# Optimization experiments

Hardware: AMD Instinct MI355X
Metric: run time of the kernel (lower is better)

Reference implementation:

```python
import jax, jax.numpy as jnp
import numpy as np

D_MODEL = 1024
NUM_HEADS = 16
D_KEY = D_MODEL // NUM_HEADS


def setup_inputs() -> dict:
    key = jax.random.key(0)
    ks = jax.random.split(key, 9)
    s = 1.0 / np.sqrt(D_MODEL)
    inp = {
        "x": jax.random.normal(ks[0], (4, 2048, D_MODEL), dtype=jnp.float32),
        "Wq": jax.random.uniform(ks[1], (D_MODEL, D_MODEL), jnp.float32, -s, s),
        "bq": jax.random.uniform(ks[2], (D_MODEL,), jnp.float32, -s, s),
        "Wk": jax.random.uniform(ks[3], (D_MODEL, D_MODEL), jnp.float32, -s, s),
        "bk": jax.random.uniform(ks[4], (D_MODEL,), jnp.float32, -s, s),
        "Wv": jax.random.uniform(ks[5], (D_MODEL, D_MODEL), jnp.float32, -s, s),
        "bv": jax.random.uniform(ks[6], (D_MODEL,), jnp.float32, -s, s),
        "Wo": jax.random.uniform(ks[7], (D_MODEL, D_MODEL), jnp.float32, -s, s),
        "bo": jax.random.uniform(ks[8], (D_MODEL,), jnp.float32, -s, s),
    }
    return inp


def reference(x, Wq, bq, Wk, bk, Wv, bv, Wo, bo):
    B, S, D = x.shape
    H, Dk = NUM_HEADS, D_KEY
    # QKV projections (torch Linear: x @ W.T + b; here W stored as [in,out])
    q = (x @ Wq + bq).reshape(B, S, H, Dk).transpose(0, 2, 1, 3)  # [B,H,S,Dk]
    k = (x @ Wk + bk).reshape(B, S, H, Dk).transpose(0, 2, 1, 3)
    v = (x @ Wv + bv).reshape(B, S, H, Dk).transpose(0, 2, 1, 3)
    logits = jnp.einsum("bhqd,bhkd->bhqk", q, k) / jnp.sqrt(jnp.float32(Dk))
    causal = jnp.triu(jnp.ones((S, S), dtype=bool), k=1)  # True above diagonal
    logits = jnp.where(causal, -jnp.inf, logits)
    attn = jax.nn.softmax(logits, axis=-1)
    out = jnp.einsum("bhqk,bhkd->bhqd", attn, v)  # [B,H,S,Dk]
    out = out.transpose(0, 2, 1, 3).reshape(B, S, D)
    return out @ Wo + bo
```

## Files before the change

### kernel.cpp

```cpp
#include <hip/hip_runtime.h>
#include <hip/hip_bf16.h>

#define DEVI __device__ __forceinline__

typedef __attribute__((ext_vector_type(8))) __bf16 bf16x8;
typedef __attribute__((ext_vector_type(4))) float f32x4;
typedef __attribute__((ext_vector_type(16))) float f32x16;
typedef __attribute__((ext_vector_type(8))) unsigned short ushort8;
typedef __attribute__((ext_vector_type(4))) int i32x4;

constexpr int D_MODEL = 1024;
constexpr int NHEAD   = 16;
constexpr int SEQ     = 2048;
constexpr int BATCH   = 4;
constexpr int MTOK    = BATCH * SEQ;

DEVI unsigned short f2bf(float x) {
  __hip_bfloat16 h = __float2bfloat16(x);
  return __builtin_bit_cast(unsigned short, h);
}

DEVI bf16x8 ld_bf8(const unsigned short* p) {
  ushort8 u = *reinterpret_cast<const ushort8*>(p);
  return __builtin_bit_cast(bf16x8, u);
}

DEVI void gload_lds16(const void* g, void* l) {
  __builtin_amdgcn_global_load_lds(
      (const __attribute__((address_space(1))) void*)g,
      (__attribute__((address_space(3))) void*)l, 16, 0, 0);
}

DEVI int cvtpk(float a, float b) {
  int r;
  asm("v_cvt_pk_bf16_f32 %0, %1, %2" : "=v"(r) : "v"(a), "v"(b));
  return r;
}
DEVI void pswap(int& a, int& b) {
  asm volatile("v_permlane32_swap_b32 %0, %1" : "+v"(a), "+v"(b));
}
DEVI float xhalf_sum(float x) { return x + __shfl_xor(x, 32, 64); }

DEVI float tree16sum(const float* p) {
  float a = p[0] + p[1], b = p[2] + p[3], c = p[4] + p[5], d = p[6] + p[7];
  float e = p[8] + p[9], f = p[10] + p[11], g = p[12] + p[13], h = p[14] + p[15];
  a += b; c += d; e += f; g += h;
  return (a + c) + (e + g);
}
DEVI bf16x8 mk_frag(const float* p, int off) {
  int w0 = cvtpk(p[off + 0], p[off + 1]);
  int w1 = cvtpk(p[off + 2], p[off + 3]);
  int w2 = cvtpk(p[off + 4], p[off + 5]);
  int w3 = cvtpk(p[off + 6], p[off + 7]);
  pswap(w0, w2);
  pswap(w1, w3);
  i32x4 v{w0, w1, w2, w3};
  return __builtin_bit_cast(bf16x8, v);
}

__global__ void prep_kernel(const float* __restrict__ x, unsigned short* __restrict__ xb,
                            const float* __restrict__ Wq, const float* __restrict__ Wk,
                            const float* __restrict__ Wv, const float* __restrict__ Wo,
                            unsigned short* __restrict__ Wtq, unsigned short* __restrict__ Wtk,
                            unsigned short* __restrict__ Wtv, unsigned short* __restrict__ Wto) {
  const int z = blockIdx.z;
  if (z >= 4) {
    const int bid = (z - 4) * 256 + blockIdx.y * 16 + blockIdx.x;
    const float4* in4 = reinterpret_cast<const float4*>(x);
    ushort4* out4 = reinterpret_cast<ushort4*>(xb);
#pragma unroll
    for (int j = 0; j < 16; ++j) {
      const int i4 = bid * 4096 + j * 256 + threadIdx.x;
      float4 v = in4[i4];
      ushort4 o;
      o.x = f2bf(v.x); o.y = f2bf(v.y); o.z = f2bf(v.z); o.w = f2bf(v.w);
      out4[i4] = o;
    }
    return;
  }
  __shared__ float tile[64][65];
  const float* W = z == 0 ? Wq : z == 1 ? Wk : z == 2 ? Wv : Wo;
  unsigned short* Wt = z == 0 ? Wtq : z == 1 ? Wtk : z == 2 ? Wtv : Wto;
  const int k0 = blockIdx.x * 64, n0 = blockIdx.y * 64;
  const int tx = threadIdx.x & 63, ty = threadIdx.x >> 6;
  for (int r = ty; r < 64; r += 4)
    tile[r][tx] = W[(size_t)(k0 + r) * D_MODEL + n0 + tx];
  __syncthreads();
  for (int r = ty; r < 64; r += 4)
    Wt[(size_t)(n0 + r) * D_MODEL + k0 + tx] = f2bf(tile[tx][r]);
}

__global__ __launch_bounds__(256) void gemm128(
    const unsigned short* __restrict__ A,
    const unsigned short* __restrict__ Bt,
    const float* __restrict__ bias,
    void* __restrict__ outp, int mode, float scale) {
  constexpr int K = 1024, N = 1024, KT = K / 64;
  __shared__ __align__(16) unsigned short As[2][128 * 64];
  __shared__ __align__(16) unsigned short Bs[2][128 * 64];
  const int t = threadIdx.x;
  const int w = t >> 6, l = t & 63;
  const int bid2 = ((blockIdx.x & 7) << 6) | (blockIdx.x >> 3);
  const int bm = bid2 >> 3, bn = bid2 & 7;
  const int m0 = bm * 128, n0 = bn * 128;
  const int wm = (w >> 1) * 64, wn = (w & 1) * 64;
  const int lr = l & 15, lg = l >> 4;

  f32x4 acc[4][4] = {};

  auto stage = [&](int kt, int buf) {
    const int k0 = kt * 64;
#pragma unroll
    for (int p = 0; p < 4; ++p) {
      const int seg = p * 4 + w;
      const int row = seg * 8 + (l >> 3);
      const int c = (l & 7) ^ (row & 7);
      gload_lds16(A + (size_t)(m0 + row) * K + k0 + c * 8, &As[buf][seg * 512]);
      gload_lds16(Bt + (size_t)(n0 + row) * K + k0 + c * 8, &Bs[buf][seg * 512]);
    }
  };

  stage(0, 0);
  __syncthreads();

  for (int kt = 0; kt < KT; ++kt) {
    const int cur = kt & 1;
    if (kt + 1 < KT) {
      stage(kt + 1, cur ^ 1);
      asm volatile("s_waitcnt vmcnt(8)" ::: "memory");
    } else {
      asm volatile("s_waitcnt vmcnt(0)" ::: "memory");
    }
    __builtin_amdgcn_sched_barrier(0);
    __builtin_amdgcn_s_barrier();
#pragma unroll
    for (int ks = 0; ks < 2; ++ks) {
      bf16x8 af[4], bfr[4];
      const int kk = lg + ks * 4;
#pragma unroll
      for (int i = 0; i < 4; ++i) {
        const int rowA = wm + i * 16 + lr;
        af[i] = ld_bf8(&As[cur][rowA * 64 + ((kk ^ (rowA & 7)) * 8)]);
        const int rowB = wn + i * 16 + lr;
        bfr[i] = ld_bf8(&Bs[cur][rowB * 64 + ((kk ^ (rowB & 7)) * 8)]);
      }
#pragma unroll
      for (int mi = 0; mi < 4; ++mi)
#pragma unroll
        for (int ni = 0; ni < 4; ++ni)
          acc[mi][ni] = __builtin_amdgcn_mfma_f32_16x16x32_bf16(
              af[mi], bfr[ni], acc[mi][ni], 0, 0, 0);
    }
    __builtin_amdgcn_sched_barrier(0);
    __builtin_amdgcn_s_barrier();
  }

#pragma unroll
  for (int ni = 0; ni < 4; ++ni) {
    const int n = n0 + wn + ni * 16 + lr;
    const float bv = bias[n];
#pragma unroll
    for (int mi = 0; mi < 4; ++mi) {
#pragma unroll
      for (int r = 0; r < 4; ++r) {
        const int m = m0 + wm + mi * 16 + lg * 4 + r;
        const float v = (acc[mi][ni][r] + bv) * scale;
        if (mode == 2) {
          ((float*)outp)[(size_t)m * N + n] = v;
        } else {
          const int b = m >> 11, s = m & 2047, h = n >> 6, dk = n & 63;
          unsigned short* o = (unsigned short*)outp;
          if (mode == 0)
            o[(((size_t)(b * NHEAD + h) * SEQ + s) << 6) + dk] = f2bf(v);
          else
            o[(((size_t)(b * NHEAD + h) << 6) + dk) * SEQ + s] = f2bf(v);
        }
      }
    }
  }
}

__global__ __launch_bounds__(256) void attn_kernel(
    const unsigned short* __restrict__ Q,
    const unsigned short* __restrict__ Kt,
    const unsigned short* __restrict__ Vt,
    unsigned short* __restrict__ Oa) {
  __shared__ __align__(16) unsigned short Ks[2][64 * 64];
  __shared__ __align__(16) unsigned short Vs[2][64 * 64];
  const int t = threadIdx.x, w = t >> 6, l = t & 63;
  const int bid = blockIdx.x;
  const int tix = bid >> 6;
  const int tk = tix >> 2, tg = tix & 3;
  const int qt = tk == 0 ? 15 - tg : tk == 1 ? 8 + tg : tk == 2 ? 4 + tg : 3 - tg;
  const int bh = bid & 63;
  const int l31 = l & 31, hi = l >> 5;
  const int jcnt = 2 * qt + 2;
  const int q0w = qt * 128 + w * 32;
  const int qg = q0w + l31;

  const unsigned short* Qb = Q + ((size_t)bh * SEQ + qg) * 64;
  bf16x8 qf[4];
#pragma unroll
  for (int ks = 0; ks < 4; ++ks)
    qf[ks] = ld_bf8(Qb + ks * 16 + hi * 8);

  f32x16 psum = {};
  f32x16 oacc[2] = {};

  auto stage = [&](int jtile, int buf) {
#pragma unroll
    for (int i = 0; i < 2; ++i) {
      const int seg = w * 2 + i;
      const int row = seg * 8 + (l >> 3);
      const int cg = (l & 7) ^ (row & 7);
      gload_lds16(Kt + (((size_t)bh * SEQ + jtile * 64 + row) << 6) + cg * 8,
                  &Ks[buf][seg * 512]);
      gload_lds16(Vt + ((size_t)bh * 64 + row) * SEQ + jtile * 64 + cg * 8,
                  &Vs[buf][seg * 512]);
    }
  };

  stage(0, 0);
  __syncthreads();

  for (int jt = 0; jt < jcnt; ++jt) {
    const int cur = jt & 1;
    if (jt + 1 < jcnt) {
      stage(jt + 1, cur ^ 1);
      asm volatile("s_waitcnt vmcnt(4)" ::: "memory");
    } else {
      asm volatile("s_waitcnt vmcnt(0)" ::: "memory");
    }
    __builtin_amdgcn_sched_barrier(0);
    __builtin_amdgcn_s_barrier();
    const int j0 = jt * 64;
    const bool active = (j0 <= q0w + 31);
    if (active) {
      const bool live1 = (j0 < q0w);
      const bool maskT = (j0 + 32 >= q0w);

      f32x16 s0 = {}, s1 = {};
      __builtin_amdgcn_s_setprio(1);
#pragma unroll
      for (int ks = 0; ks < 4; ++ks) {
        bf16x8 kf = ld_bf8(&Ks[cur][l31 * 64 + ((((ks << 1) | hi) ^ (l31 & 7)) << 3)]);
        s0 = __builtin_amdgcn_mfma_f32_32x32x16_bf16(kf, qf[ks], s0, 0, 0, 0);
      }
      if (live1) {
#pragma unroll
        for (int ks = 0; ks < 4; ++ks) {
          const int r1 = 32 + l31;
          bf16x8 kf = ld_bf8(&Ks[cur][r1 * 64 + ((((ks << 1) | hi) ^ (r1 & 7)) << 3)]);
          s1 = __builtin_amdgcn_mfma_f32_32x32x16_bf16(kf, qf[ks], s1, 0, 0, 0);
        }
      }
      __builtin_amdgcn_s_setprio(0);

      float p0[16];
      if (maskT) {
#pragma unroll
        for (int r = 0; r < 16; ++r) {
          const int key = j0 + (r & 3) + ((r >> 2) << 3) + (hi << 2);
          p0[r] = (key > qg) ? 0.f : exp2f(s0[r]);
        }
      } else {
#pragma unroll
        for (int r = 0; r < 16; ++r) p0[r] = exp2f(s0[r]);
      }
#pragma unroll
      for (int r = 0; r < 16; ++r) psum[r] += p0[r];

      __builtin_amdgcn_s_setprio(1);
#pragma unroll
      for (int ks = 0; ks < 2; ++ks) {
        bf16x8 pf = mk_frag(p0, ks * 8);
#pragma unroll
        for (int dt = 0; dt < 2; ++dt) {
          const int rv = dt * 32 + l31;
          bf16x8 vf = ld_bf8(&Vs[cur][rv * 64 + ((((ks << 1) | hi) ^ (rv & 7)) << 3)]);
          oacc[dt] = __builtin_amdgcn_mfma_f32_32x32x16_bf16(vf, pf, oacc[dt], 0, 0, 0);
        }
      }
      __builtin_amdgcn_s_setprio(0);

      if (live1) {
        float p1[16];
        if (maskT) {
#pragma unroll
          for (int r = 0; r < 16; ++r) {
            const int key = j0 + 32 + (r & 3) + ((r >> 2) << 3) + (hi << 2);
            p1[r] = (key > qg) ? 0.f : exp2f(s1[r]);
          }
        } else {
#pragma unroll
          for (int r = 0; r < 16; ++r) p1[r] = exp2f(s1[r]);
        }
#pragma unroll
        for (int r = 0; r < 16; ++r) psum[r] += p1[r];
        __builtin_amdgcn_s_setprio(1);
#pragma unroll
        for (int ks = 0; ks < 2; ++ks) {
          bf16x8 pf = mk_frag(p1, ks * 8);
#pragma unroll
          for (int dt = 0; dt < 2; ++dt) {
            const int rv = dt * 32 + l31;
            bf16x8 vf = ld_bf8(&Vs[cur][rv * 64 + (((((ks + 2) << 1) | hi) ^ (rv & 7)) << 3)]);
            oacc[dt] = __builtin_amdgcn_mfma_f32_32x32x16_bf16(vf, pf, oacc[dt], 0, 0, 0);
          }
        }
        __builtin_amdgcn_s_setprio(0);
      }
    }
    __builtin_amdgcn_sched_barrier(0);
    __builtin_amdgcn_s_barrier();
  }

  float pa[16];
#pragma unroll
  for (int r = 0; r < 16; ++r) pa[r] = psum[r];
  const float l_ = xhalf_sum(tree16sum(pa));
  const float rinv = 1.f / l_;
  const int b = bh >> 4, h = bh & 15;
  unsigned short* orow = Oa + ((size_t)(b * SEQ) + qg) * D_MODEL + h * 64;
#pragma unroll
  for (int dt = 0; dt < 2; ++dt)
#pragma unroll
    for (int g = 0; g < 4; ++g) {
      const int d = dt * 32 + g * 8 + hi * 4;
      uint2 u;
      u.x = (unsigned)cvtpk(oacc[dt][g * 4 + 0] * rinv, oacc[dt][g * 4 + 1] * rinv);
      u.y = (unsigned)cvtpk(oacc[dt][g * 4 + 2] * rinv, oacc[dt][g * 4 + 3] * rinv);
      *reinterpret_cast<uint2*>(orow + d) = u;
    }
}

extern "C" void kernel_launch(void* const* d_in, const int* in_sizes, int n_in,
                              void* d_out, int out_size, void* d_ws, size_t ws_size,
                              hipStream_t stream) {
  const float* x  = (const float*)d_in[0];
  const float* Wq = (const float*)d_in[1];
  const float* bq = (const float*)d_in[2];
  const float* Wk = (const float*)d_in[3];
  const float* bk = (const float*)d_in[4];
  const float* Wv = (const float*)d_in[5];
  const float* bv = (const float*)d_in[6];
  const float* Wo = (const float*)d_in[7];
  const float* bo = (const float*)d_in[8];

  char* ws = (char*)d_ws;
  unsigned short* xb    = (unsigned short*)(ws + 0);
  unsigned short* attnb = (unsigned short*)(ws + 0);
  unsigned short* wtq   = (unsigned short*)(ws + 16777216);
  unsigned short* wtk   = (unsigned short*)(ws + 18874368);
  unsigned short* wtv   = (unsigned short*)(ws + 20971520);
  unsigned short* wto   = (unsigned short*)(ws + 23068672);
  unsigned short* Qw    = (unsigned short*)(ws + 25165824);
  unsigned short* Kw    = (unsigned short*)(ws + 41943040);
  unsigned short* Vtw   = (unsigned short*)(ws + 58720256);

  prep_kernel<<<dim3(16, 16, 6), 256, 0, stream>>>(x, xb, Wq, Wk, Wv, Wo,
                                                   wtq, wtk, wtv, wto);

  gemm128<<<512, 256, 0, stream>>>(xb, wtq, bq, (void*)Qw, 0, 0.18033688011112042f);
  gemm128<<<512, 256, 0, stream>>>(xb, wtk, bk, (void*)Kw, 0, 1.0f);
  gemm128<<<512, 256, 0, stream>>>(xb, wtv, bv, (void*)Vtw, 1, 1.0f);

  attn_kernel<<<1024, 256, 0, stream>>>(Qw, Kw, Vtw, attnb);

  gemm128<<<512, 256, 0, stream>>>(attnb, wto, bo, d_out, 2, 1.0f);
}
```

Baseline: 192.6 us.

## Split KV range of long causal query tiles across blocks with finalize merge

Query tiles 11-15 now have their key range split in two. Extra blocks compute the first half of the keys and write unnormalized partial outputs and row sums to workspace. The original blocks compute the second half directly into the output buffer. A new finalize kernel adds the two partials and divides by the combined denominator. This shortens the longest blocks in the causal attention grid so load across CUs is more even. The cost is an extra kernel launch, partial-result traffic, and bf16 rounding of the unnormalized partials.

```diff
diff --git a/kernel.cpp b/kernel.cpp
--- a/kernel.cpp
+++ b/kernel.cpp
@@ -18,6 +18,9 @@
 DEVI unsigned short f2bf(float x) {
   __hip_bfloat16 h = __float2bfloat16(x);
   return __builtin_bit_cast(unsigned short, h);
+}
+DEVI float bf2f(unsigned short u) {
+  return __bfloat162float(__builtin_bit_cast(__hip_bfloat16, u));
 }
 
 DEVI bf16x8 ld_bf8(const unsigned short* p) {
@@ -184,17 +187,29 @@
     const unsigned short* __restrict__ Q,
     const unsigned short* __restrict__ Kt,
     const unsigned short* __restrict__ Vt,
-    unsigned short* __restrict__ Oa) {
+    unsigned short* __restrict__ Oa,
+    unsigned short* __restrict__ pAo,
+    float* __restrict__ pAl,
+    float* __restrict__ pBl) {
   __shared__ __align__(16) unsigned short Ks[2][64 * 64];
   __shared__ __align__(16) unsigned short Vs[2][64 * 64];
   const int t = threadIdx.x, w = t >> 6, l = t & 63;
   const int bid = blockIdx.x;
-  const int tix = bid >> 6;
-  const int tk = tix >> 2, tg = tix & 3;
-  const int qt = tk == 0 ? 15 - tg : tk == 1 ? 8 + tg : tk == 2 ? 4 + tg : 3 - tg;
-  const int bh = bid & 63;
   const int l31 = l & 31, hi = l >> 5;
-  const int jcnt = 2 * qt + 2;
+
+  int qt, bh, jt0, jt1, mode, sidx = 0;
+  if (bid < 320) {
+    sidx = bid; qt = 11 + (bid >> 6); bh = bid & 63;
+    jt0 = 0; jt1 = qt + 1; mode = 2;
+  } else {
+    const int jb = bid - 320;
+    const int tix = jb >> 6; bh = jb & 63;
+    const int tk = tix >> 2, tg = tix & 3;
+    qt = tk == 0 ? 15 - tg : tk == 1 ? 8 + tg : tk == 2 ? 4 + tg : 3 - tg;
+    jt1 = 2 * qt + 2;
+    if (qt >= 11) { jt0 = qt + 1; mode = 1; sidx = (qt - 11) * 64 + bh; }
+    else { jt0 = 0; mode = 0; }
+  }
   const int q0w = qt * 128 + w * 32;
   const int qg = q0w + l31;
 
@@ -220,12 +235,14 @@
     }
   };
 
-  stage(0, 0);
+  stage(jt0, 0);
   __syncthreads();
 
-  for (int jt = 0; jt < jcnt; ++jt) {
-    const int cur = jt & 1;
-    if (jt + 1 < jcnt) {
+  const int jn = jt1 - jt0;
+  for (int jc = 0; jc < jn; ++jc) {
+    const int jt = jt0 + jc;
+    const int cur = jc & 1;
+    if (jc + 1 < jn) {
       stage(jt + 1, cur ^ 1);
       asm volatile("s_waitcnt vmcnt(4)" ::: "memory");
     } else {
@@ -319,19 +336,62 @@
 #pragma unroll
   for (int r = 0; r < 16; ++r) pa[r] = psum[r];
   const float l_ = xhalf_sum(tree16sum(pa));
-  const float rinv = 1.f / l_;
   const int b = bh >> 4, h = bh & 15;
-  unsigned short* orow = Oa + ((size_t)(b * SEQ) + qg) * D_MODEL + h * 64;
-#pragma unroll
-  for (int dt = 0; dt < 2; ++dt)
-#pragma unroll
-    for (int g = 0; g < 4; ++g) {
-      const int d = dt * 32 + g * 8 + hi * 4;
-      uint2 u;
-      u.x = (unsigned)cvtpk(oacc[dt][g * 4 + 0] * rinv, oacc[dt][g * 4 + 1] * rinv);
-      u.y = (unsigned)cvtpk(oacc[dt][g * 4 + 2] * rinv, oacc[dt][g * 4 + 3] * rinv);
-      *reinterpret_cast<uint2*>(orow + d) = u;
-    }
+  const int rloc = w * 32 + l31;
+
+  if (mode == 0) {
+    const float rinv = 1.f / l_;
+    unsigned short* orow = Oa + ((size_t)(b * SEQ) + qg) * D_MODEL + h * 64;
+#pragma unroll
+    for (int dt = 0; dt < 2; ++dt)
+#pragma unroll
+      for (int g = 0; g < 4; ++g) {
+        const int d = dt * 32 + g * 8 + hi * 4;
+        uint2 u;
+        u.x = (unsigned)cvtpk(oacc[dt][g * 4 + 0] * rinv, oacc[dt][g * 4 + 1] * rinv);
+        u.y = (unsigned)cvtpk(oacc[dt][g * 4 + 2] * rinv, oacc[dt][g * 4 + 3] * rinv);
+        *reinterpret_cast<uint2*>(orow + d) = u;
+      }
+  } else {
+    unsigned short* obase = (mode == 1)
+        ? Oa + ((size_t)(b * SEQ) + qg) * D_MODEL + h * 64
+        : pAo + (size_t)sidx * 8192 + rloc * 64;
+#pragma unroll
+    for (int dt = 0; dt < 2; ++dt)
+#pragma unroll
+      for (int g = 0; g < 4; ++g) {
+        const int d = dt * 32 + g * 8 + hi * 4;
+        uint2 u;
+        u.x = (unsigned)cvtpk(oacc[dt][g * 4 + 0], oacc[dt][g * 4 + 1]);
+        u.y = (unsigned)cvtpk(oacc[dt][g * 4 + 2], oacc[dt][g * 4 + 3]);
+        *reinterpret_cast<uint2*>(obase + d) = u;
+      }
+    if (hi == 0) {
+      float* lbuf = (mode == 1) ? pBl : pAl;
+      lbuf[sidx * 128 + rloc] = l_;
+    }
+  }
+}
+
+__global__ __launch_bounds__(256) void finalize_kernel(
+    unsigned short* __restrict__ Oa,
+    const unsigned short* __restrict__ pAo,
+    const float* __restrict__ pAl,
+    const float* __restrict__ pBl) {
+  const int sidx = blockIdx.x;
+  const int qt = 11 + (sidx >> 6), bh = sidx & 63;
+  const int b = bh >> 4, h = bh & 15;
+#pragma unroll
+  for (int i = 0; i < 32; ++i) {
+    const int e = i * 256 + threadIdx.x;
+    const int r = e >> 6, d = e & 63;
+    const int s = qt * 128 + r;
+    const size_t ai = ((size_t)(b * SEQ + s)) * D_MODEL + h * 64 + d;
+    const float ob = bf2f(Oa[ai]);
+    const float oa = bf2f(pAo[(size_t)sidx * 8192 + e]);
+    const float denom = pAl[sidx * 128 + r] + pBl[sidx * 128 + r];
+    Oa[ai] = f2bf((ob + oa) / denom);
+  }
 }
 
 extern "C" void kernel_launch(void* const* d_in, const int* in_sizes, int n_in,
@@ -357,6 +417,9 @@
   unsigned short* Qw    = (unsigned short*)(ws + 25165824);
   unsigned short* Kw    = (unsigned short*)(ws + 41943040);
   unsigned short* Vtw   = (unsigned short*)(ws + 58720256);
+  unsigned short* pAo = (unsigned short*)(ws + 16777216);
+  float*          pAl = (float*)(ws + 22020096);
+  float*          pBl = (float*)(ws + 22183936);
 
   prep_kernel<<<dim3(16, 16, 6), 256, 0, stream>>>(x, xb, Wq, Wk, Wv, Wo,
                                                    wtq, wtk, wtv, wto);
@@ -365,7 +428,8 @@
   gemm128<<<512, 256, 0, stream>>>(xb, wtk, bk, (void*)Kw, 0, 1.0f);
   gemm128<<<512, 256, 0, stream>>>(xb, wtv, bv, (void*)Vtw, 1, 1.0f);
 
-  attn_kernel<<<1024, 256, 0, stream>>>(Qw, Kw, Vtw, attnb);
+  attn_kernel<<<1344, 256, 0, stream>>>(Qw, Kw, Vtw, attnb, pAo, pAl, pBl);
+  finalize_kernel<<<320, 256, 0, stream>>>(attnb, pAo, pAl, pBl);
 
   gemm128<<<512, 256, 0, stream>>>(attnb, wto, bo, d_out, 2, 1.0f);
 }
```

Result: slower. 217.6 us (+13.0%).
